# Performance work log

Hardware: AMD Instinct MI355X
Metric: run time of the kernel (lower is better)

Reference implementation:

```python
import jax, jax.numpy as jnp
import numpy as np

B, T = 128, 64
N_IN, N_HID, N_OUT = 1024, 4096, 1024
TAU = 0.9          # init_tau, used for both LIF decay and output accumulation
THRESH = 0.5       # spike threshold (HeavisideBoxcar)
SUBTHRESH = 0.5    # boxcar surrogate half-width
REC_SCALE = 0.1    # 0.1 * hidden_spike @ recurrent

@jax.custom_vjp
def spike_fn(v):
    # Heaviside forward, boxcar surrogate backward
    return (v >= THRESH).astype(v.dtype)

def _spike_fwd(v):
    return spike_fn(v), v

def _spike_bwd(v, g):
    return (g * (jnp.abs(v - THRESH) <= SUBTHRESH).astype(g.dtype),)

spike_fn.defvjp(_spike_fwd, _spike_bwd)


def setup_inputs() -> dict:
    key = jax.random.key(0)
    k_x, k_fc1, k_rec, k_out = jax.random.split(key, 4)
    x = jax.random.uniform(k_x, (B, T, N_IN), dtype=jnp.float32)
    # torch Linear weights stored here already transposed to [in, out]
    W_fc1 = jax.random.uniform(k_fc1, (N_IN, N_HID), dtype=jnp.float32,
                               minval=-1.0, maxval=1.0) / np.sqrt(N_IN)
    W_rec = jax.random.uniform(k_rec, (N_HID, N_HID), dtype=jnp.float32) / np.sqrt(N_HID)
    W_rec = W_rec * (1.0 - jnp.eye(N_HID, dtype=jnp.float32))  # fill_diagonal_(0)
    W_out = jax.random.uniform(k_out, (N_HID, N_OUT), dtype=jnp.float32,
                               minval=-1.0, maxval=1.0) / np.sqrt(N_HID)
    return {"x": x, "W_fc1": W_fc1, "W_rec": W_rec, "W_out": W_out}


def reference(x, W_fc1, W_rec, W_out):
    # x: [B, T, n_in] -> outputs: [B, T, n_out]
    def step(carry, x_t):
        h_mem, h_spk, o_mem = carry
        inp = x_t @ W_fc1 + REC_SCALE * (h_spk @ W_rec)
        h_mem = TAU * h_mem * (1.0 - h_spk) + inp   # decay + hard reset + input
        h_spk = spike_fn(h_mem)
        o_mem = TAU * o_mem + h_spk @ W_out          # Accumulate_node
        return (h_mem, h_spk, o_mem), o_mem

    zH = jnp.zeros((x.shape[0], N_HID), dtype=x.dtype)
    zO = jnp.zeros((x.shape[0], N_OUT), dtype=x.dtype)
    xs = jnp.swapaxes(x, 0, 1)  # [T, B, n_in]
    _, outs = jax.lax.scan(step, (zH, zH, zO), xs)
    return jnp.swapaxes(outs, 0, 1)  # [B, T, n_out]
```

## Files before the change

kernel.cpp:

```cpp
#include <hip/hip_runtime.h>
#include <stdint.h>

#define B_SZ 128
#define T_SZ 64
#define N_IN 1024
#define N_HID 4096
#define N_OUT 1024
#define TAU 0.9f
#define THRESH 0.5f
#define REC_SCALE 0.1f
#define S_DENSE 6
#define KSPLIT 8

typedef __attribute__((ext_vector_type(8))) short sh8;
typedef __attribute__((ext_vector_type(4))) float f32x4;
typedef __attribute__((ext_vector_type(4))) unsigned short ush4;
typedef __attribute__((ext_vector_type(8))) unsigned short ush8;

__device__ __forceinline__ unsigned short f2bf_rn(float f) {
    unsigned u = __float_as_uint(f);
    unsigned r = (u + 0x7FFFu + ((u >> 16) & 1u)) >> 16;
    return (unsigned short)r;
}
__device__ __forceinline__ float bf2f(unsigned short h) {
    return __uint_as_float((unsigned)h << 16);
}
__device__ __forceinline__ void gload_lds16(const void* g, void* l) {
    __builtin_amdgcn_global_load_lds(
        (const __attribute__((address_space(1))) void*)g,
        (__attribute__((address_space(3))) void*)l, 16, 0, 0);
}
__device__ __forceinline__ unsigned pack4(unsigned a) {
    a &= 0x0F0F0F0Fu;
    a = (a | (a >> 4)) & 0x00FF00FFu;
    a = (a | (a >> 8)) & 0x0000FFFFu;
    return a;
}

__global__ void zero_state_kernel(float* p, int n) {
    int i = blockIdx.x * blockDim.x + threadIdx.x;
    int stride = gridDim.x * blockDim.x;
    for (; i < n; i += stride) p[i] = 0.0f;
}

__global__ __launch_bounds__(256)
void f32_to_bf16_kernel(const float* __restrict__ src,
                        unsigned short* __restrict__ dst, int n4) {
    int i = blockIdx.x * blockDim.x + threadIdx.x;
    int stride = gridDim.x * blockDim.x;
    for (; i < n4; i += stride) {
        float4 v = ((const float4*)src)[i];
        ush4 o;
        o[0] = f2bf_rn(v.x); o[1] = f2bf_rn(v.y);
        o[2] = f2bf_rn(v.z); o[3] = f2bf_rn(v.w);
        ((ush4*)dst)[i] = o;
    }
}

__global__ __launch_bounds__(256)
void transpose_bf16_kernel(const float* __restrict__ W,
                           unsigned short* __restrict__ WT, int R, int C) {
    __shared__ float ts[64][65];
    int tid = threadIdx.x;
    int c0 = blockIdx.x * 64;
    int r0 = blockIdx.y * 64;
    #pragma unroll
    for (int rr = 0; rr < 16; ++rr) {
        int r = rr * 4 + (tid >> 6);
        int c = tid & 63;
        ts[r][c] = W[(size_t)(r0 + r) * C + c0 + c];
    }
    __syncthreads();
    #pragma unroll
    for (int rr = 0; rr < 16; ++rr) {
        int c = rr * 4 + (tid >> 6);
        int r = tid & 63;
        WT[(size_t)(c0 + c) * R + r0 + r] = f2bf_rn(ts[r][c]);
    }
}

__global__ __launch_bounds__(256)
void colsum_bf16_kernel(const unsigned short* __restrict__ WrecB,
                        const unsigned short* __restrict__ WoutB,
                        float* __restrict__ cs_rec, float* __restrict__ cs_out) {
    __shared__ float part[4][64];
    int tid = threadIdx.x;
    int c = tid & 63, q = tid >> 6;
    int col = blockIdx.x * 64 + c;
    float s = 0.f;
    if (col < N_HID) {
        const unsigned short* p = WrecB + col + (size_t)q * 1024 * N_HID;
        for (int j = 0; j < 1024; ++j) s += bf2f(p[(size_t)j * N_HID]);
    } else {
        int o = col - N_HID;
        const unsigned short* p = WoutB + o + (size_t)q * 1024 * N_OUT;
        for (int j = 0; j < 1024; ++j) s += bf2f(p[(size_t)j * N_OUT]);
    }
    part[q][c] = s;
    __syncthreads();
    if (tid < 64) {
        float tot = part[0][tid] + part[1][tid] + part[2][tid] + part[3][tid];
        int col2 = blockIdx.x * 64 + tid;
        if (col2 < N_HID) cs_rec[col2] = tot;
        else              cs_out[col2 - N_HID] = tot;
    }
}

__global__ __launch_bounds__(256)
void convert_x_kernel(const float* __restrict__ x, unsigned short* __restrict__ Ax,
                      int t0, int Tc) {
    int total4 = B_SZ * Tc * (N_IN / 4);
    int i = blockIdx.x * blockDim.x + threadIdx.x;
    int stride = gridDim.x * blockDim.x;
    for (; i < total4; i += stride) {
        int m = i >> 8;
        int c4 = i & 255;
        int b = m / Tc, tl = m - b * Tc;
        float4 v = *(const float4*)(x + ((size_t)(b * T_SZ + t0 + tl) * N_IN) + c4 * 4);
        ush4 hi, lo;
        float f[4] = {v.x, v.y, v.z, v.w};
        #pragma unroll
        for (int j = 0; j < 4; ++j) {
            unsigned short h = f2bf_rn(f[j]);
            hi[j] = h;
            lo[j] = f2bf_rn(f[j] - bf2f(h));
        }
        unsigned short* row = Ax + (size_t)m * 2048;
        *(ush4*)(row + c4 * 4)        = hi;
        *(ush4*)(row + 1024 + c4 * 4) = lo;
    }
}

__global__ __launch_bounds__(256)
void convert_w_kernel(const float* __restrict__ W, unsigned short* __restrict__ Bt) {
    __shared__ float ts[32][65];
    int tid = threadIdx.x;
    int k0 = blockIdx.x * 32;
    int n0 = blockIdx.y * 64;
    #pragma unroll
    for (int rr = 0; rr < 8; ++rr) {
        int kl = (tid >> 6) * 8 + rr;
        int nl = tid & 63;
        ts[kl][nl] = W[(size_t)(k0 + kl) * N_HID + n0 + nl];
    }
    __syncthreads();
    #pragma unroll
    for (int rr = 0; rr < 8; ++rr) {
        int nl = (tid >> 5) + rr * 8;
        int kl = tid & 31;
        float v = ts[kl][nl];
        unsigned short h = f2bf_rn(v);
        unsigned short l = f2bf_rn(v - bf2f(h));
        unsigned short* row = Bt + (size_t)(n0 + nl) * 2048;
        row[k0 + kl]        = h;
        row[1024 + k0 + kl] = l;
    }
}

__global__ __launch_bounds__(256)
void fc1_mfma_kernel(const unsigned short* __restrict__ A,
                     const unsigned short* __restrict__ Bt,
                     float* __restrict__ C) {
    __shared__ __attribute__((aligned(16))) unsigned short As[128 * 32];
    __shared__ __attribute__((aligned(16))) unsigned short Bs[128 * 32];
    const int tid = threadIdx.x;
    const int lane = tid & 63;
    const int wave = tid >> 6;
    const int wm = (wave >> 1) * 64;
    const int wn = (wave & 1) * 64;
    const int quad = lane >> 4, l16 = lane & 15;
    const int m0 = blockIdx.y * 128, n0 = blockIdx.x * 128;

    const unsigned short* aptr[2];
    const unsigned short* bptr[2];
    unsigned short* alds[2];
    unsigned short* blds[2];
    #pragma unroll
    for (int i = 0; i < 2; ++i) {
        int idx = tid + 256 * i;
        int row = idx >> 2, cg = idx & 3;
        aptr[i] = A  + (size_t)(m0 + row) * 2048 + cg * 8;
        bptr[i] = Bt + (size_t)(n0 + row) * 2048 + cg * 8;
        alds[i] = As + idx * 8;
        blds[i] = Bs + idx * 8;
    }

    f32x4 acc[4][4] = {};
    for (int kt = 0; kt < 96; ++kt) {
        int kk = kt * 32;
        int ak = (kk < 2048) ? kk : kk - 2048;
        int bk = (kk < 1024) ? kk : kk - 1024;
        __syncthreads();
        #pragma unroll
        for (int i = 0; i < 2; ++i) {
            gload_lds16(aptr[i] + ak, alds[i]);
            gload_lds16(bptr[i] + bk, blds[i]);
        }
        __syncthreads();
        sh8 af[4], bf[4];
        #pragma unroll
        for (int mt = 0; mt < 4; ++mt)
            af[mt] = *(const sh8*)&As[(wm + mt * 16 + l16) * 32 + quad * 8];
        #pragma unroll
        for (int nt = 0; nt < 4; ++nt)
            bf[nt] = *(const sh8*)&Bs[(wn + nt * 16 + l16) * 32 + quad * 8];
        #pragma unroll
        for (int mt = 0; mt < 4; ++mt)
            #pragma unroll
            for (int nt = 0; nt < 4; ++nt)
                acc[mt][nt] = __builtin_amdgcn_mfma_f32_16x16x32_bf16(
                    af[mt], bf[nt], acc[mt][nt], 0, 0, 0);
    }
    #pragma unroll
    for (int mt = 0; mt < 4; ++mt)
        #pragma unroll
        for (int nt = 0; nt < 4; ++nt) {
            int col = n0 + wn + nt * 16 + l16;
            #pragma unroll
            for (int r = 0; r < 4; ++r) {
                int m = m0 + wm + mt * 16 + quad * 4 + r;
                C[(size_t)m * N_HID + col] = acc[mt][nt][r];
            }
        }
}

__global__ __launch_bounds__(256)
void spk_gemm_kernel(const unsigned short* __restrict__ A,
                     const unsigned short* __restrict__ BT,
                     float* __restrict__ part, int Nfull) {
    __shared__ __attribute__((aligned(16))) unsigned short As[128 * 32];
    __shared__ __attribute__((aligned(16))) unsigned short Bs[128 * 32];
    const int tid = threadIdx.x;
    const int lane = tid & 63;
    const int wave = tid >> 6;
    const int wm = (wave >> 1) * 64;
    const int wn = (wave & 1) * 64;
    const int quad = lane >> 4, l16 = lane & 15;
    const int n0 = blockIdx.x * 128;
    const int k0 = blockIdx.y * (N_HID / KSPLIT);

    const unsigned short* aptr[2];
    const unsigned short* bptr[2];
    unsigned short* alds[2];
    unsigned short* blds[2];
    #pragma unroll
    for (int i = 0; i < 2; ++i) {
        int idx = tid + 256 * i;
        int row = idx >> 2, cg = idx & 3;
        aptr[i] = A  + (size_t)row * N_HID + k0 + cg * 8;
        bptr[i] = BT + (size_t)(n0 + row) * N_HID + k0 + cg * 8;
        alds[i] = As + idx * 8;
        blds[i] = Bs + idx * 8;
    }

    f32x4 acc[4][4] = {};
    for (int kt = 0; kt < (N_HID / KSPLIT) / 32; ++kt) {
        int kk = kt * 32;
        __syncthreads();
        #pragma unroll
        for (int i = 0; i < 2; ++i) {
            gload_lds16(aptr[i] + kk, alds[i]);
            gload_lds16(bptr[i] + kk, blds[i]);
        }
        __syncthreads();
        sh8 af[4], bf[4];
        #pragma unroll
        for (int mt = 0; mt < 4; ++mt)
            af[mt] = *(const sh8*)&As[(wm + mt * 16 + l16) * 32 + quad * 8];
        #pragma unroll
        for (int nt = 0; nt < 4; ++nt)
            bf[nt] = *(const sh8*)&Bs[(wn + nt * 16 + l16) * 32 + quad * 8];
        #pragma unroll
        for (int mt = 0; mt < 4; ++mt)
            #pragma unroll
            for (int nt = 0; nt < 4; ++nt)
                acc[mt][nt] = __builtin_amdgcn_mfma_f32_16x16x32_bf16(
                    af[mt], bf[nt], acc[mt][nt], 0, 0, 0);
    }
    float* pout = part + (size_t)blockIdx.y * 128 * Nfull;
    #pragma unroll
    for (int mt = 0; mt < 4; ++mt)
        #pragma unroll
        for (int nt = 0; nt < 4; ++nt) {
            int col = n0 + wn + nt * 16 + l16;
            #pragma unroll
            for (int r = 0; r < 4; ++r) {
                int m = wm + mt * 16 + quad * 4 + r;
                pout[(size_t)m * Nfull + col] = acc[mt][nt][r];
            }
        }
}

__global__ __launch_bounds__(1024)
void transient_update_kernel(const float* __restrict__ inp,
                             const float* __restrict__ rec_part,
                             const float* __restrict__ out_part,
                             float* __restrict__ h_mem,
                             float* __restrict__ o_mem,
                             unsigned short* __restrict__ spk,
                             unsigned long long* __restrict__ maskg,
                             float* __restrict__ out,
                             int t_glob, int Tc, int has_rec, int has_out) {
    __shared__ __attribute__((aligned(16))) unsigned char spkb[1024];
    const int b = blockIdx.x;
    const int t = threadIdx.x;
    const int lane = t & 63;
    const int wave = t >> 6;

    if (has_out) {
        float s = 0.f;
        #pragma unroll
        for (int ks = 0; ks < KSPLIT; ++ks)
            s += out_part[(size_t)ks * B_SZ * N_OUT + (size_t)b * N_OUT + t];
        float o = TAU * o_mem[(size_t)b * N_OUT + t] + s;
        o_mem[(size_t)b * N_OUT + t] = o;
        out[((size_t)b * T_SZ + (t_glob - 1)) * N_OUT + t] = o;
    }

    float rec[4] = {0.f, 0.f, 0.f, 0.f};
    if (has_rec) {
        #pragma unroll
        for (int ks = 0; ks < KSPLIT; ++ks) {
            float4 p = *(const float4*)(rec_part + (size_t)ks * B_SZ * N_HID
                                        + (size_t)b * N_HID + 4 * t);
            rec[0] += p.x; rec[1] += p.y; rec[2] += p.z; rec[3] += p.w;
        }
    }

    unsigned short* sp = spk + (size_t)b * N_HID + 4 * t;
    ush4 prev = *(const ush4*)sp;
    float4 iv = *(const float4*)(inp + ((size_t)b * Tc + t_glob) * N_HID + 4 * t);
    float ivv[4] = {iv.x, iv.y, iv.z, iv.w};
    float* hp = h_mem + (size_t)b * N_HID + 4 * t;
    float hv[4] = {hp[0], hp[1], hp[2], hp[3]};
    ush4 news;
    unsigned nib = 0;
    #pragma unroll
    for (int k = 0; k < 4; ++k) {
        float spf = bf2f(prev[k]);
        float v = TAU * hv[k] * (1.0f - spf) + (ivv[k] + REC_SCALE * rec[k]);
        hp[k] = v;
        bool s = (v >= THRESH);
        news[k] = s ? (unsigned short)0x3F80 : (unsigned short)0;
        nib |= (s ? 1u : 0u) << k;
    }
    *(ush4*)sp = news;
    spkb[t] = (unsigned char)nib;
    __syncthreads();
    if (wave == 0) {
        uint4 q = *(const uint4*)&spkb[lane * 16];
        unsigned w0 = pack4(q.x) | (pack4(q.y) << 16);
        unsigned w1 = pack4(q.z) | (pack4(q.w) << 16);
        maskg[b * 64 + lane] = (unsigned long long)w0
                             | ((unsigned long long)w1 << 32);
    }
}

__device__ __forceinline__ void build_list_core(unsigned long long w,
                                                unsigned short* list,
                                                int* sh_n, int* sh_inact,
                                                int lane) {
    int tot = __builtin_popcountll(w);
    #pragma unroll
    for (int d = 32; d > 0; d >>= 1) tot += __shfl_xor(tot, d, 64);
    int inact = tot > (N_HID / 2);
    unsigned long long wsel = inact ? ~w : w;
    int c = __builtin_popcountll(wsel);
    int scan = c;
    #pragma unroll
    for (int d = 1; d < 64; d <<= 1) {
        int v = __shfl_up(scan, d, 64);
        if (lane >= d) scan += v;
    }
    int off = scan - c;
    while (wsel) {
        int bpos = __builtin_ctzll(wsel);
        list[off++] = (unsigned short)(lane * 64 + bpos);
        wsel &= wsel - 1;
    }
    if (lane == 0) {
        *sh_n = inact ? (N_HID - tot) : tot;
        *sh_inact = inact;
    }
}

__global__ __launch_bounds__(1024, 4)
void rsnn_step_kernel(const float* __restrict__ inp,
                      const unsigned short* __restrict__ WrecB,
                      const unsigned short* __restrict__ WoutB,
                      const float* __restrict__ cs_rec,
                      const float* __restrict__ cs_out,
                      const float* __restrict__ out_part,
                      float* __restrict__ h_mem_g,
                      float* __restrict__ o_mem_g,
                      unsigned long long* __restrict__ mask_g,
                      float* __restrict__ out,
                      int t0, int Tc, int tloc0, int nsteps, int do_accum) {
    __shared__ unsigned long long mask[64];
    __shared__ __attribute__((aligned(16))) unsigned short list[N_HID];
    __shared__ __attribute__((aligned(16))) unsigned char spk[1024];
    __shared__ int sh_n;
    __shared__ int sh_inact;

    const int b = blockIdx.x;
    const int t = threadIdx.x;
    const int lane = t & 63;
    const int wave = t >> 6;

    float hm[4], csr[4];
    #pragma unroll
    for (int k = 0; k < 4; ++k) {
        hm[k]  = h_mem_g[(size_t)b * N_HID + 4 * t + k];
        csr[k] = cs_rec[4 * t + k];
    }
    float om  = o_mem_g[(size_t)b * N_OUT + t];
    float cso = cs_out[t];
    if (do_accum) {
        float s = 0.f;
        #pragma unroll
        for (int ks = 0; ks < KSPLIT; ++ks)
            s += out_part[(size_t)ks * B_SZ * N_OUT + (size_t)b * N_OUT + t];
        om = TAU * om + s;
        out[((size_t)b * T_SZ + (t0 + tloc0 - 1)) * N_OUT + t] = om;
    }
    if (t < 64) mask[t] = mask_g[b * 64 + t];
    __syncthreads();

    float spf[4];
    {
        unsigned long long w = mask[t >> 4];
        int sh = 4 * (t & 15);
        #pragma unroll
        for (int k = 0; k < 4; ++k)
            spf[k] = (float)((w >> (sh + k)) & 1ULL);
    }
    if (wave == 0) build_list_core(mask[lane], list, &sh_n, &sh_inact, lane);
    __syncthreads();

    const unsigned short* Wb = WrecB + 4 * t;
    const unsigned short* Wo = WoutB + t;

    for (int tl = 0; tl < nsteps; ++tl) {
        int n = sh_n, inact = sh_inact;
        float a[8][4] = {};
        int i = 0;
        for (; i + 8 <= n; i += 8) {
            ush8 jv = *(const ush8*)&list[i];
            #pragma unroll
            for (int r = 0; r < 8; ++r) {
                uint2 v = *(const uint2*)(Wb + (size_t)jv[r] * N_HID);
                a[r][0] += __uint_as_float(v.x << 16);
                a[r][1] += __uint_as_float(v.x & 0xFFFF0000u);
                a[r][2] += __uint_as_float(v.y << 16);
                a[r][3] += __uint_as_float(v.y & 0xFFFF0000u);
            }
        }
        for (; i < n; ++i) {
            uint2 v = *(const uint2*)(Wb + (size_t)list[i] * N_HID);
            a[0][0] += __uint_as_float(v.x << 16);
            a[0][1] += __uint_as_float(v.x & 0xFFFF0000u);
            a[0][2] += __uint_as_float(v.y << 16);
            a[0][3] += __uint_as_float(v.y & 0xFFFF0000u);
        }
        float racc[4];
        #pragma unroll
        for (int k = 0; k < 4; ++k)
            racc[k] = ((a[0][k] + a[1][k]) + (a[2][k] + a[3][k]))
                    + ((a[4][k] + a[5][k]) + (a[6][k] + a[7][k]));

        float4 iv = *(const float4*)(inp + ((size_t)b * Tc + tloc0 + tl) * N_HID + 4 * t);
        float ivv[4] = {iv.x, iv.y, iv.z, iv.w};
        unsigned nib = 0;
        #pragma unroll
        for (int k = 0; k < 4; ++k) {
            float rec = REC_SCALE * (inact ? (csr[k] - racc[k]) : racc[k]);
            float v = TAU * hm[k] * (1.0f - spf[k]) + (ivv[k] + rec);
            hm[k] = v;
            bool s = (v >= THRESH);
            spf[k] = s ? 1.0f : 0.0f;
            nib |= (s ? 1u : 0u) << k;
        }
        __syncthreads();
        spk[t] = (unsigned char)nib;
        __syncthreads();
        if (wave == 0) {
            uint4 q = *(const uint4*)&spk[lane * 16];
            unsigned w0 = pack4(q.x) | (pack4(q.y) << 16);
            unsigned w1 = pack4(q.z) | (pack4(q.w) << 16);
            unsigned long long w = (unsigned long long)w0
                                 | ((unsigned long long)w1 << 32);
            mask[lane] = w;
            build_list_core(w, list, &sh_n, &sh_inact, lane);
        }
        __syncthreads();

        int n2 = sh_n; inact = sh_inact;
        float o8[8] = {};
        i = 0;
        for (; i + 16 <= n2; i += 16) {
            ush8 j0 = *(const ush8*)&list[i];
            ush8 j1 = *(const ush8*)&list[i + 8];
            #pragma unroll
            for (int r = 0; r < 8; ++r) o8[r] += bf2f(Wo[(size_t)j0[r] * N_OUT]);
            #pragma unroll
            for (int r = 0; r < 8; ++r) o8[r] += bf2f(Wo[(size_t)j1[r] * N_OUT]);
        }
        for (; i + 8 <= n2; i += 8) {
            ush8 j0 = *(const ush8*)&list[i];
            #pragma unroll
            for (int r = 0; r < 8; ++r) o8[r] += bf2f(Wo[(size_t)j0[r] * N_OUT]);
        }
        for (; i < n2; ++i) o8[0] += bf2f(Wo[(size_t)list[i] * N_OUT]);
        float oacc = ((o8[0] + o8[1]) + (o8[2] + o8[3]))
                   + ((o8[4] + o8[5]) + (o8[6] + o8[7]));
        float contrib = inact ? (cso - oacc) : oacc;
        om = TAU * om + contrib;
        out[((size_t)b * T_SZ + (t0 + tloc0 + tl)) * N_OUT + t] = om;
    }

    #pragma unroll
    for (int k = 0; k < 4; ++k)
        h_mem_g[(size_t)b * N_HID + 4 * t + k] = hm[k];
    o_mem_g[(size_t)b * N_OUT + t] = om;
    __syncthreads();
    if (t < 64) mask_g[b * 64 + t] = mask[t];
}

extern "C" void kernel_launch(void* const* d_in, const int* in_sizes, int n_in,
                              void* d_out, int out_size, void* d_ws, size_t ws_size,
                              hipStream_t stream) {
    const float* x    = (const float*)d_in[0];
    const float* Wfc1 = (const float*)d_in[1];
    const float* Wrec = (const float*)d_in[2];
    const float* Wout = (const float*)d_in[3];
    float* out = (float*)d_out;

    float* h_mem = (float*)d_ws;
    float* o_mem = h_mem + B_SZ * N_HID;
    unsigned long long* maskg =
        (unsigned long long*)(o_mem + B_SZ * N_OUT);
    float* cs_rec = (float*)(maskg + B_SZ * 64);
    float* cs_out = cs_rec + N_HID;
    unsigned short* WrecB = (unsigned short*)(cs_out + N_OUT);
    unsigned short* WoutB = WrecB + (size_t)N_HID * N_HID;
    unsigned short* WrecT = WoutB + (size_t)N_HID * N_OUT;
    unsigned short* WoutT = WrecT + (size_t)N_HID * N_HID;
    unsigned short* Bt    = WoutT + (size_t)N_OUT * N_HID;
    unsigned short* spk   = Bt + (size_t)N_HID * 2048;
    float* rec_part = (float*)(spk + (size_t)B_SZ * N_HID);
    float* out_part = rec_part + (size_t)KSPLIT * B_SZ * N_HID;
    unsigned short* Ax = (unsigned short*)(out_part + (size_t)KSPLIT * B_SZ * N_OUT);

    size_t fixed_bytes = (size_t)(B_SZ * N_HID + B_SZ * N_OUT) * 4
                       + (size_t)B_SZ * 64 * 8
                       + (size_t)(N_HID + N_OUT) * 4
                       + 2 * (size_t)N_HID * N_HID * 2
                       + 2 * (size_t)N_HID * N_OUT * 2
                       + (size_t)N_HID * 2048 * 2
                       + (size_t)B_SZ * N_HID * 2
                       + (size_t)KSPLIT * B_SZ * (N_HID + N_OUT) * 4;
    int Tc = 64;
    while (Tc > 8 &&
           fixed_bytes + (size_t)Tc * (B_SZ * 2048 * 2 + B_SZ * N_HID * 4) > ws_size)
        Tc >>= 1;
    float* inp_chunk = (float*)(Ax + (size_t)B_SZ * Tc * 2048);

    int state_floats = B_SZ * N_HID + B_SZ * N_OUT + B_SZ * 64 * 2;
    zero_state_kernel<<<256, 256, 0, stream>>>(h_mem, state_floats);
    f32_to_bf16_kernel<<<2048, 256, 0, stream>>>(Wrec, WrecB, N_HID * N_HID / 4);
    f32_to_bf16_kernel<<<1024, 256, 0, stream>>>(Wout, WoutB, N_HID * N_OUT / 4);
    transpose_bf16_kernel<<<dim3(N_HID / 64, N_HID / 64), 256, 0, stream>>>(
        Wrec, WrecT, N_HID, N_HID);
    transpose_bf16_kernel<<<dim3(N_OUT / 64, N_HID / 64), 256, 0, stream>>>(
        Wout, WoutT, N_HID, N_OUT);
    colsum_bf16_kernel<<<80, 256, 0, stream>>>(WrecB, WoutB, cs_rec, cs_out);
    convert_w_kernel<<<dim3(32, 64), 256, 0, stream>>>(Wfc1, Bt);

    for (int t0 = 0; t0 < T_SZ; t0 += Tc) {
        convert_x_kernel<<<2048, 256, 0, stream>>>(x, Ax, t0, Tc);
        fc1_mfma_kernel<<<dim3(N_HID / 128, Tc), 256, 0, stream>>>(Ax, Bt, inp_chunk);

        if (t0 == 0) {
            for (int tg = 0; tg < S_DENSE; ++tg) {
                transient_update_kernel<<<B_SZ, 1024, 0, stream>>>(
                    inp_chunk, rec_part, out_part, h_mem, o_mem, spk, maskg, out,
                    tg, Tc, tg > 0, tg > 0);
                spk_gemm_kernel<<<dim3(N_OUT / 128, KSPLIT), 256, 0, stream>>>(
                    spk, WoutT, out_part, N_OUT);
                if (tg + 1 < S_DENSE)
                    spk_gemm_kernel<<<dim3(N_HID / 128, KSPLIT), 256, 0, stream>>>(
                        spk, WrecT, rec_part, N_HID);
            }
            rsnn_step_kernel<<<B_SZ, 1024, 0, stream>>>(
                inp_chunk, WrecB, WoutB, cs_rec, cs_out, out_part,
                h_mem, o_mem, maskg, out,
                t0, Tc, S_DENSE, Tc - S_DENSE, 1);
        } else {
            rsnn_step_kernel<<<B_SZ, 1024, 0, stream>>>(
                inp_chunk, WrecB, WoutB, cs_rec, cs_out, out_part,
                h_mem, o_mem, maskg, out,
                t0, Tc, 0, Tc, 0);
        }
    }
}
```

Before: 841.4 us.

## Fuse dense transient steps into one cooperative kernel with grid syncs

Replaces the per-step sequence of update kernel plus two spike GEMM launches for the first dense timesteps with a single cooperative kernel of 256 blocks. Within each step the blocks run the LIF update, then grid.sync(), then the recurrent and output GEMM tiles, then grid.sync() again. This removes about 17 kernel launches and their launch gaps. In exchange, the update phase now uses 256 threads per batch row and 128 blocks sit idle during it, and the design depends on every block being co-resident for the grid barrier.

Measured after the change: 1.483 ms. 1.76x slower.

```diff
diff --git a/kernel.cpp b/kernel.cpp
--- a/kernel.cpp
+++ b/kernel.cpp
@@ -1,5 +1,8 @@
 #include <hip/hip_runtime.h>
+#include <hip/hip_cooperative_groups.h>
 #include <stdint.h>
+
+namespace cg = cooperative_groups;
 
 #define B_SZ 128
 #define T_SZ 64
@@ -224,20 +227,19 @@
         }
 }
 
-__global__ __launch_bounds__(256)
-void spk_gemm_kernel(const unsigned short* __restrict__ A,
-                     const unsigned short* __restrict__ BT,
-                     float* __restrict__ part, int Nfull) {
-    __shared__ __attribute__((aligned(16))) unsigned short As[128 * 32];
-    __shared__ __attribute__((aligned(16))) unsigned short Bs[128 * 32];
-    const int tid = threadIdx.x;
+__device__ __forceinline__ void spk_tile_gemm(const unsigned short* __restrict__ A,
+                                              const unsigned short* __restrict__ BT,
+                                              float* __restrict__ part, int Nfull,
+                                              int nt, int ks,
+                                              unsigned short* As, unsigned short* Bs,
+                                              int tid) {
     const int lane = tid & 63;
     const int wave = tid >> 6;
     const int wm = (wave >> 1) * 64;
     const int wn = (wave & 1) * 64;
     const int quad = lane >> 4, l16 = lane & 15;
-    const int n0 = blockIdx.x * 128;
-    const int k0 = blockIdx.y * (N_HID / KSPLIT);
+    const int n0 = nt * 128;
+    const int k0 = ks * (N_HID / KSPLIT);
 
     const unsigned short* aptr[2];
     const unsigned short* bptr[2];
@@ -268,91 +270,119 @@
         for (int mt = 0; mt < 4; ++mt)
             af[mt] = *(const sh8*)&As[(wm + mt * 16 + l16) * 32 + quad * 8];
         #pragma unroll
-        for (int nt = 0; nt < 4; ++nt)
-            bf[nt] = *(const sh8*)&Bs[(wn + nt * 16 + l16) * 32 + quad * 8];
+        for (int nt2 = 0; nt2 < 4; ++nt2)
+            bf[nt2] = *(const sh8*)&Bs[(wn + nt2 * 16 + l16) * 32 + quad * 8];
         #pragma unroll
         for (int mt = 0; mt < 4; ++mt)
             #pragma unroll
-            for (int nt = 0; nt < 4; ++nt)
-                acc[mt][nt] = __builtin_amdgcn_mfma_f32_16x16x32_bf16(
-                    af[mt], bf[nt], acc[mt][nt], 0, 0, 0);
-    }
-    float* pout = part + (size_t)blockIdx.y * 128 * Nfull;
+            for (int nt2 = 0; nt2 < 4; ++nt2)
+                acc[mt][nt2] = __builtin_amdgcn_mfma_f32_16x16x32_bf16(
+                    af[mt], bf[nt2], acc[mt][nt2], 0, 0, 0);
+    }
+    float* pout = part + (size_t)ks * 128 * Nfull;
     #pragma unroll
     for (int mt = 0; mt < 4; ++mt)
         #pragma unroll
-        for (int nt = 0; nt < 4; ++nt) {
-            int col = n0 + wn + nt * 16 + l16;
+        for (int nt2 = 0; nt2 < 4; ++nt2) {
+            int col = n0 + wn + nt2 * 16 + l16;
             #pragma unroll
             for (int r = 0; r < 4; ++r) {
                 int m = wm + mt * 16 + quad * 4 + r;
-                pout[(size_t)m * Nfull + col] = acc[mt][nt][r];
+                pout[(size_t)m * Nfull + col] = acc[mt][nt2][r];
             }
         }
 }
 
-__global__ __launch_bounds__(1024)
-void transient_update_kernel(const float* __restrict__ inp,
-                             const float* __restrict__ rec_part,
-                             const float* __restrict__ out_part,
-                             float* __restrict__ h_mem,
-                             float* __restrict__ o_mem,
-                             unsigned short* __restrict__ spk,
-                             unsigned long long* __restrict__ maskg,
-                             float* __restrict__ out,
-                             int t_glob, int Tc, int has_rec, int has_out) {
+__global__ __launch_bounds__(256, 2)
+void transient_coop_kernel(const float* __restrict__ inp,
+                           const unsigned short* __restrict__ WrecT,
+                           const unsigned short* __restrict__ WoutT,
+                           float* __restrict__ rec_part,
+                           float* __restrict__ out_part,
+                           float* __restrict__ h_mem,
+                           float* __restrict__ o_mem,
+                           unsigned short* __restrict__ spk,
+                           unsigned long long* __restrict__ maskg,
+                           float* __restrict__ out,
+                           int Tc) {
+    __shared__ __attribute__((aligned(16))) unsigned short As[128 * 32];
+    __shared__ __attribute__((aligned(16))) unsigned short Bs[128 * 32];
     __shared__ __attribute__((aligned(16))) unsigned char spkb[1024];
-    const int b = blockIdx.x;
-    const int t = threadIdx.x;
-    const int lane = t & 63;
-    const int wave = t >> 6;
-
-    if (has_out) {
-        float s = 0.f;
-        #pragma unroll
-        for (int ks = 0; ks < KSPLIT; ++ks)
-            s += out_part[(size_t)ks * B_SZ * N_OUT + (size_t)b * N_OUT + t];
-        float o = TAU * o_mem[(size_t)b * N_OUT + t] + s;
-        o_mem[(size_t)b * N_OUT + t] = o;
-        out[((size_t)b * T_SZ + (t_glob - 1)) * N_OUT + t] = o;
-    }
-
-    float rec[4] = {0.f, 0.f, 0.f, 0.f};
-    if (has_rec) {
-        #pragma unroll
-        for (int ks = 0; ks < KSPLIT; ++ks) {
-            float4 p = *(const float4*)(rec_part + (size_t)ks * B_SZ * N_HID
-                                        + (size_t)b * N_HID + 4 * t);
-            rec[0] += p.x; rec[1] += p.y; rec[2] += p.z; rec[3] += p.w;
-        }
-    }
-
-    unsigned short* sp = spk + (size_t)b * N_HID + 4 * t;
-    ush4 prev = *(const ush4*)sp;
-    float4 iv = *(const float4*)(inp + ((size_t)b * Tc + t_glob) * N_HID + 4 * t);
-    float ivv[4] = {iv.x, iv.y, iv.z, iv.w};
-    float* hp = h_mem + (size_t)b * N_HID + 4 * t;
-    float hv[4] = {hp[0], hp[1], hp[2], hp[3]};
-    ush4 news;
-    unsigned nib = 0;
-    #pragma unroll
-    for (int k = 0; k < 4; ++k) {
-        float spf = bf2f(prev[k]);
-        float v = TAU * hv[k] * (1.0f - spf) + (ivv[k] + REC_SCALE * rec[k]);
-        hp[k] = v;
-        bool s = (v >= THRESH);
-        news[k] = s ? (unsigned short)0x3F80 : (unsigned short)0;
-        nib |= (s ? 1u : 0u) << k;
-    }
-    *(ush4*)sp = news;
-    spkb[t] = (unsigned char)nib;
-    __syncthreads();
-    if (wave == 0) {
-        uint4 q = *(const uint4*)&spkb[lane * 16];
-        unsigned w0 = pack4(q.x) | (pack4(q.y) << 16);
-        unsigned w1 = pack4(q.z) | (pack4(q.w) << 16);
-        maskg[b * 64 + lane] = (unsigned long long)w0
-                             | ((unsigned long long)w1 << 32);
+    cg::grid_group grid = cg::this_grid();
+
+    const int bid = blockIdx.x;
+    const int tid = threadIdx.x;
+    const int lane = tid & 63;
+    const int wave = tid >> 6;
+
+    for (int tg = 0; tg < S_DENSE; ++tg) {
+        if (bid < B_SZ) {
+            const int b = bid;
+            if (tg > 0) {
+                #pragma unroll
+                for (int j = 0; j < 4; ++j) {
+                    int col = tid + 256 * j;
+                    float s = 0.f;
+                    #pragma unroll
+                    for (int ks = 0; ks < KSPLIT; ++ks)
+                        s += out_part[(size_t)ks * B_SZ * N_OUT + (size_t)b * N_OUT + col];
+                    float o = TAU * o_mem[(size_t)b * N_OUT + col] + s;
+                    o_mem[(size_t)b * N_OUT + col] = o;
+                    out[((size_t)b * T_SZ + (tg - 1)) * N_OUT + col] = o;
+                }
+            }
+            #pragma unroll
+            for (int j = 0; j < 4; ++j) {
+                int t4 = tid + 256 * j;
+                float rec[4] = {0.f, 0.f, 0.f, 0.f};
+                if (tg > 0) {
+                    #pragma unroll
+                    for (int ks = 0; ks < KSPLIT; ++ks) {
+                        float4 p = *(const float4*)(rec_part + (size_t)ks * B_SZ * N_HID
+                                                    + (size_t)b * N_HID + 4 * t4);
+                        rec[0] += p.x; rec[1] += p.y; rec[2] += p.z; rec[3] += p.w;
+                    }
+                }
+                unsigned short* sp = spk + (size_t)b * N_HID + 4 * t4;
+                ush4 prev = *(const ush4*)sp;
+                float4 iv = *(const float4*)(inp + ((size_t)b * Tc + tg) * N_HID + 4 * t4);
+                float ivv[4] = {iv.x, iv.y, iv.z, iv.w};
+                float* hp = h_mem + (size_t)b * N_HID + 4 * t4;
+                float hv[4] = {hp[0], hp[1], hp[2], hp[3]};
+                ush4 news;
+                unsigned nib = 0;
+                #pragma unroll
+                for (int k = 0; k < 4; ++k) {
+                    float spf = bf2f(prev[k]);
+                    float v = TAU * hv[k] * (1.0f - spf) + (ivv[k] + REC_SCALE * rec[k]);
+                    hp[k] = v;
+                    bool s = (v >= THRESH);
+                    news[k] = s ? (unsigned short)0x3F80 : (unsigned short)0;
+                    nib |= (s ? 1u : 0u) << k;
+                }
+                *(ush4*)sp = news;
+                spkb[t4] = (unsigned char)nib;
+            }
+            __syncthreads();
+            if (wave == 0) {
+                uint4 q = *(const uint4*)&spkb[lane * 16];
+                unsigned w0 = pack4(q.x) | (pack4(q.y) << 16);
+                unsigned w1 = pack4(q.z) | (pack4(q.w) << 16);
+                maskg[b * 64 + lane] = (unsigned long long)w0
+                                     | ((unsigned long long)w1 << 32);
+            }
+        }
+        grid.sync();
+        if (tg + 1 < S_DENSE) {
+            spk_tile_gemm(spk, WrecT, rec_part, N_HID,
+                          bid & 31, bid >> 5, As, Bs, tid);
+        }
+        if ((bid & 3) == 0) {
+            int o = bid >> 2;
+            spk_tile_gemm(spk, WoutT, out_part, N_OUT,
+                          o & 7, o >> 3, As, Bs, tid);
+        }
+        grid.sync();
     }
 }
 
@@ -581,16 +611,13 @@
         fc1_mfma_kernel<<<dim3(N_HID / 128, Tc), 256, 0, stream>>>(Ax, Bt, inp_chunk);
 
         if (t0 == 0) {
-            for (int tg = 0; tg < S_DENSE; ++tg) {
-                transient_update_kernel<<<B_SZ, 1024, 0, stream>>>(
-                    inp_chunk, rec_part, out_part, h_mem, o_mem, spk, maskg, out,
-                    tg, Tc, tg > 0, tg > 0);
-                spk_gemm_kernel<<<dim3(N_OUT / 128, KSPLIT), 256, 0, stream>>>(
-                    spk, WoutT, out_part, N_OUT);
-                if (tg + 1 < S_DENSE)
-                    spk_gemm_kernel<<<dim3(N_HID / 128, KSPLIT), 256, 0, stream>>>(
-                        spk, WrecT, rec_part, N_HID);
-            }
+            void* args[] = {(void*)&inp_chunk, (void*)&WrecT, (void*)&WoutT,
+                            (void*)&rec_part, (void*)&out_part,
+                            (void*)&h_mem, (void*)&o_mem, (void*)&spk,
+                            (void*)&maskg, (void*)&out, (void*)&Tc};
+            hipLaunchCooperativeKernel(
+                reinterpret_cast<void*>(transient_coop_kernel),
+                dim3(256), dim3(256), args, 0, stream);
             rsnn_step_kernel<<<B_SZ, 1024, 0, stream>>>(
                 inp_chunk, WrecB, WoutB, cs_rec, cs_out, out_part,
                 h_mem, o_mem, maskg, out,
```
